# Kernel tuning notes

Hardware: AMD Instinct MI355X
Metric: run time of the kernel (lower is better)

The kernel has to match this reference:

```python
import jax, jax.numpy as jnp
import numpy as np

B, S, E, H = 2, 2048, 1024, 16
D = E // H


def setup_inputs() -> dict:
    key = jax.random.key(0)
    ks = jax.random.split(key, 11)
    def lin(k):
        kw, kb = jax.random.split(k)
        bound = 1.0 / np.sqrt(E)
        W = jax.random.uniform(kw, (E, E), jnp.float32, -bound, bound)
        b = jax.random.uniform(kb, (E,), jnp.float32, -bound, bound)
        return W, b
    Wq, bq = lin(ks[0])
    Wk, bk = lin(ks[1])
    Wv, bv = lin(ks[2])
    Wo, bo = lin(ks[3])
    return {
        "query": jax.random.normal(ks[4], (B, S, E), jnp.float32),
        "key": jax.random.normal(ks[5], (B, S, E), jnp.float32),
        "value": jax.random.normal(ks[6], (B, S, E), jnp.float32),
        "Wq": Wq, "bq": bq, "Wk": Wk, "bk": bk,
        "Wv": Wv, "bv": bv, "Wo": Wo, "bo": bo,
        "is_causal": 1,
    }


def reference(query, key, value, Wq, bq, Wk, bk, Wv, bv, Wo, bo, is_causal):
    scale = D ** -0.5
    def heads(x, W, b):
        # torch Linear: x @ W.T + b, then [B,S,H,D] -> [B,H,S,D]
        y = jnp.einsum('bse,fe->bsf', x, W) + b
        return y.reshape(B, S, H, D).transpose(0, 2, 1, 3)
    q = heads(query, Wq, bq)
    k = heads(key, Wk, bk)
    v = heads(value, Wv, bv)
    scores = jnp.einsum('bhqd,bhkd->bhqk', q, k) * scale  # [B,H,S,S]
    if is_causal:
        mask = jnp.tril(jnp.ones((S, S), dtype=bool))
        scores = jnp.where(mask, scores, -jnp.inf)
    attn = jax.nn.softmax(scores, axis=-1)
    out = jnp.einsum('bhqk,bhkd->bhqd', attn, v)
    out = out.transpose(0, 2, 1, 3).reshape(B, S, E)
    return jnp.einsum('bse,fe->bsf', out, Wo) + bo
```

## Files before the change

kernel.cpp:

```cpp
#include <hip/hip_runtime.h>
#include <cstdint>
#include <cstddef>

typedef unsigned short u16;
typedef unsigned int u32;
typedef __attribute__((ext_vector_type(8))) short bf16x8;
typedef __attribute__((ext_vector_type(4))) float f32x4;
typedef __attribute__((ext_vector_type(16))) float f32x16;
typedef __attribute__((ext_vector_type(4))) u16 u16x4;
typedef __attribute__((ext_vector_type(4))) u32 u32x4;
typedef __attribute__((ext_vector_type(2))) u32 u32x2;

__device__ __forceinline__ u16 f2bf(float f) {
  u32 x = __builtin_bit_cast(u32, f);
  x += 0x7fffu + ((x >> 16) & 1u);
  return (u16)(x >> 16);
}

__device__ __forceinline__ void g2lds16(const u16* g, u16* l) {
  __builtin_amdgcn_global_load_lds(
      (const __attribute__((address_space(1))) u32*)g,
      (__attribute__((address_space(3))) u32*)l, 16, 0, 0);
}

struct CvtArgs { const float* s[7]; u16* d[7]; int n4[7]; };

__global__ __launch_bounds__(256) void cvt_all(CvtArgs a) {
  int y = blockIdx.y;
  const float4* __restrict__ src = (const float4*)a.s[y];
  u16* __restrict__ dst = a.d[y];
  int n4 = a.n4[y];
  for (int i = blockIdx.x * blockDim.x + threadIdx.x; i < n4;
       i += gridDim.x * blockDim.x) {
    float4 v = src[i];
    u16x4 o = { f2bf(v.x), f2bf(v.y), f2bf(v.z), f2bf(v.w) };
    *(u16x4*)(dst + (size_t)i * 4) = o;
  }
}

struct GemmArgs {
  const u16* A[3]; const u16* W[3]; const float* bias[3];
  void* out[3]; float scale[3]; int mode[3];
};

__global__ __launch_bounds__(256) void gemm_fused(GemmArgs ga) {
  __shared__ alignas(16) u16 As[2][128 * 32];
  __shared__ alignas(16) u16 Bs[2][128 * 32];
  const int z = blockIdx.z;
  const u16* __restrict__ A = ga.A[z];
  const u16* __restrict__ W = ga.W[z];
  const int tid = threadIdx.x;
  const int lane = tid & 63;
  const int w = tid >> 6;
  const int lo4 = lane & 15, hi2 = lane >> 4;
  const int l = (int)blockIdx.x + 8 * (int)blockIdx.y;
  const int wl = (l & 7) * 32 + (l >> 3);
  const int m0 = (wl >> 3) * 128;
  const int n0 = (wl & 7) * 128;
  const int wr = w >> 1, wc = w & 1;

  f32x4 acc[4][4] = {};

  auto stage = [&](int kt, int buf) {
    const int k0 = kt * 32;
#pragma unroll
    for (int i = 0; i < 2; ++i) {
      int c = (i * 4 + w) * 64 + lane;
      int r = c >> 2;
      int q = (c & 3) ^ ((r >> 1) & 3);
      g2lds16(A + (size_t)(m0 + r) * 1024 + k0 + q * 8, As[buf] + (i * 4 + w) * 512);
      g2lds16(W + (size_t)(n0 + r) * 1024 + k0 + q * 8, Bs[buf] + (i * 4 + w) * 512);
    }
  };

  stage(0, 0);
  stage(1, 1);
  for (int kt = 0; kt < 32; ++kt) {
    const int cur = kt & 1;
    asm volatile("s_waitcnt vmcnt(4)" ::: "memory");
    __builtin_amdgcn_s_barrier();
    bf16x8 af[4], bfr[4];
#pragma unroll
    for (int i = 0; i < 4; ++i) {
      int r = wr * 64 + i * 16 + lo4;
      int q = hi2 ^ ((r >> 1) & 3);
      af[i] = *(const bf16x8*)(As[cur] + r * 32 + q * 8);
    }
#pragma unroll
    for (int j = 0; j < 4; ++j) {
      int r = wc * 64 + j * 16 + lo4;
      int q = hi2 ^ ((r >> 1) & 3);
      bfr[j] = *(const bf16x8*)(Bs[cur] + r * 32 + q * 8);
    }
#pragma unroll
    for (int i = 0; i < 4; ++i)
#pragma unroll
      for (int j = 0; j < 4; ++j)
        acc[i][j] = __builtin_amdgcn_mfma_f32_16x16x32_bf16(af[i], bfr[j], acc[i][j], 0, 0, 0);
    __builtin_amdgcn_s_barrier();
    stage(kt + 2 < 32 ? kt + 2 : kt, cur);
  }
  asm volatile("s_waitcnt vmcnt(0)" ::: "memory");

  const float* __restrict__ bias = ga.bias[z];
  const float cs = ga.scale[z];
  const int mode = ga.mode[z];
#pragma unroll
  for (int j = 0; j < 4; ++j) {
    int n = n0 + wc * 64 + j * 16 + lo4;
    float bv = bias[n];
#pragma unroll
    for (int i = 0; i < 4; ++i) {
#pragma unroll
      for (int rg = 0; rg < 4; ++rg) {
        int m = m0 + wr * 64 + i * 16 + hi2 * 4 + rg;
        float v = (acc[i][j][rg] + bv) * cs;
        if (mode == 2) {
          ((float*)ga.out[z])[(size_t)m * 1024 + n] = v;
        } else {
          int b = m >> 11, s = m & 2047, h = n >> 6, d = n & 63;
          size_t addr = (mode == 0)
            ? ((size_t)(b * 16 + h) * 2048 + s) * 64 + d
            : ((size_t)(b * 16 + h) * 64 + d) * 2048 + s;
          ((u16*)ga.out[z])[addr] = f2bf(v);
        }
      }
    }
  }
}

__global__ __launch_bounds__(256, 2) void attn_kernel(
    const u16* __restrict__ Q, const u16* __restrict__ K,
    const u16* __restrict__ Vt, u16* __restrict__ Out,
    const int* __restrict__ causal_p) {
  __shared__ alignas(16) u16 Ks[2][2][64 * 64];
  __shared__ alignas(16) u16 Vs[2][2][64 * 64];
  __shared__ float ml2[512];
  const int tid = threadIdx.x, lane = tid & 63, w = tid >> 6;
  const int wg = w >> 1, wv = w & 1;
  const int ql = lane & 31, hi = lane >> 5;
  const int bx = (int)blockIdx.x, by = (int)blockIdx.y;
  const int bh = (bx & 7) * 4 + (by >> 3);
  const int slot = ((bx >> 3) << 3) | (by & 7);
  const int causal = *causal_p;
  const u16* Qb = Q + (size_t)bh * 2048 * 64;
  const u16* Kb = K + (size_t)bh * 2048 * 64;
  const u16* Vb = Vt + (size_t)bh * 64 * 2048;
  const int batch = bh >> 4, h = bh & 15;

  auto stageKV = [&](int jt, int buf) {
#pragma unroll
    for (int i = 0; i < 4; ++i) {
      int c = i * 128 + wv * 64 + lane;
      int r = c >> 3;
      int q = (c & 7) ^ (r & 7);
      g2lds16(Kb + (size_t)(jt * 64 + r) * 64 + q * 8, Ks[wg][buf] + (i * 128 + wv * 64) * 8);
      g2lds16(Vb + (size_t)r * 2048 + jt * 64 + q * 8, Vs[wg][buf] + (i * 128 + wv * 64) * 8);
    }
  };

  float* Od = (float*)&Ks[0][0][0];
  const int li = wv * 64 + lane;

  for (int seg = 0; seg < 2; ++seg) {
    const int qt = seg ? 31 - slot : slot;
    const int qrow = qt * 64 + wv * 32 + ql;

    bf16x8 qf[4];
#pragma unroll
    for (int dsl = 0; dsl < 4; ++dsl)
      qf[dsl] = *(const bf16x8*)(Qb + (size_t)qrow * 64 + dsl * 16 + hi * 8);

    const int nt = causal ? (qt + 1) : 32;
    const int U = (nt + 1) >> 1;

    stageKV(wg, 0);
    stageKV(wg + 2, 1);

    float m_r = -1e30f, l_r = 0.f;
    f32x16 o0 = {}, o1 = {};

    for (int u = 0; u < U; ++u) {
      const int jt = 2 * u + wg;
      const int cur = u & 1;
      asm volatile("s_waitcnt vmcnt(8)" ::: "memory");
      __builtin_amdgcn_s_barrier();

      if (jt < nt) {
        f32x16 s0 = {}, s1 = {};
#pragma unroll
        for (int dsl = 0; dsl < 4; ++dsl) {
          int cc = dsl * 2 + hi;
          bf16x8 k0 = *(const bf16x8*)(Ks[wg][cur] + ql * 64 + ((cc ^ (ql & 7)) * 8));
          bf16x8 k1 = *(const bf16x8*)(Ks[wg][cur] + (32 + ql) * 64 + ((cc ^ (ql & 7)) * 8));
          s0 = __builtin_amdgcn_mfma_f32_32x32x16_bf16(k0, qf[dsl], s0, 0, 0, 0);
          s1 = __builtin_amdgcn_mfma_f32_32x32x16_bf16(k1, qf[dsl], s1, 0, 0, 0);
        }

        if (causal && jt == qt) {
#pragma unroll
          for (int rg = 0; rg < 16; ++rg) {
            int kof = jt * 64 + 8 * (rg >> 2) + (rg & 3) + 4 * hi;
            s0[rg] = (kof > qrow) ? -1e30f : s0[rg];
            s1[rg] = (kof + 32 > qrow) ? -1e30f : s1[rg];
          }
        }

        float pm = fmaxf(s0[0], s1[0]);
#pragma unroll
        for (int rg = 1; rg < 16; ++rg) pm = fmaxf(pm, fmaxf(s0[rg], s1[rg]));
        pm = fmaxf(pm, __shfl_xor(pm, 32));
        if (!__all(pm <= m_r + 8.f)) {
          float mn = fmaxf(m_r, pm);
          float corr = exp2f(m_r - mn);
          m_r = mn; l_r *= corr;
#pragma unroll
          for (int rg = 0; rg < 16; ++rg) { o0[rg] *= corr; o1[rg] *= corr; }
        }
        float sum = 0.f;
#pragma unroll
        for (int rg = 0; rg < 16; ++rg) { s0[rg] = exp2f(s0[rg] - m_r); sum += s0[rg]; }
#pragma unroll
        for (int rg = 0; rg < 16; ++rg) { s1[rg] = exp2f(s1[rg] - m_r); sum += s1[rg]; }
        sum += __shfl_xor(sum, 32);
        l_r += sum;

#pragma unroll
        for (int s = 0; s < 4; ++s) {
          const f32x16& p = (s >= 2) ? s1 : s0;
          const int base = 8 * (s & 1);
          u32 A0, A1, B0, B1;
          asm("v_cvt_pk_bf16_f32 %0, %1, %2" : "=v"(A0) : "v"(p[base + 0]), "v"(p[base + 1]));
          asm("v_cvt_pk_bf16_f32 %0, %1, %2" : "=v"(A1) : "v"(p[base + 2]), "v"(p[base + 3]));
          asm("v_cvt_pk_bf16_f32 %0, %1, %2" : "=v"(B0) : "v"(p[base + 4]), "v"(p[base + 5]));
          asm("v_cvt_pk_bf16_f32 %0, %1, %2" : "=v"(B1) : "v"(p[base + 6]), "v"(p[base + 7]));
          asm volatile("v_permlane32_swap_b32 %0, %1" : "+v"(A0), "+v"(B0));
          asm volatile("v_permlane32_swap_b32 %0, %1" : "+v"(A1), "+v"(B1));
          u32x4 pw = {A0, A1, B0, B1};
          bf16x8 pf = __builtin_bit_cast(bf16x8, pw);
#pragma unroll
          for (int df = 0; df < 2; ++df) {
            int rr = df * 32 + ql;
            bf16x8 vf = *(const bf16x8*)(Vs[wg][cur] + rr * 64 + (((s * 2 + hi) ^ (rr & 7)) * 8));
            if (df) o1 = __builtin_amdgcn_mfma_f32_32x32x16_bf16(vf, pf, o1, 0, 0, 0);
            else    o0 = __builtin_amdgcn_mfma_f32_32x32x16_bf16(vf, pf, o0, 0, 0, 0);
          }
        }
      }
      __builtin_amdgcn_s_barrier();
      stageKV(u + 2 < U ? jt + 4 : jt, cur);
    }
    asm volatile("s_waitcnt vmcnt(0)" ::: "memory");
    __syncthreads();

    if (wg == 1) {
#pragma unroll
      for (int rg = 0; rg < 16; ++rg) {
        Od[li * 33 + rg]      = o0[rg];
        Od[li * 33 + 16 + rg] = o1[rg];
      }
      ml2[li * 3 + 0] = m_r;
      ml2[li * 3 + 1] = l_r;
    }
    __syncthreads();
    if (wg == 0) {
      float m_b = ml2[li * 3 + 0];
      float l_b = ml2[li * 3 + 1];
      float mn = fmaxf(m_r, m_b);
      float ca = exp2f(m_r - mn), cb = exp2f(m_b - mn);
      float rl = 1.f / (l_r * ca + l_b * cb);
      u16* orow = Out + ((size_t)(batch * 2048 + qrow)) * 1024 + h * 64;
#pragma unroll
      for (int df = 0; df < 2; ++df) {
        const f32x16& oo = df ? o1 : o0;
        const float* Op = &Od[li * 33 + df * 16];
#pragma unroll
        for (int b2 = 0; b2 < 4; ++b2) {
          u32 w0, w1;
          float v0 = (oo[4 * b2 + 0] * ca + Op[4 * b2 + 0] * cb) * rl;
          float v1 = (oo[4 * b2 + 1] * ca + Op[4 * b2 + 1] * cb) * rl;
          float v2 = (oo[4 * b2 + 2] * ca + Op[4 * b2 + 2] * cb) * rl;
          float v3 = (oo[4 * b2 + 3] * ca + Op[4 * b2 + 3] * cb) * rl;
          asm("v_cvt_pk_bf16_f32 %0, %1, %2" : "=v"(w0) : "v"(v0), "v"(v1));
          asm("v_cvt_pk_bf16_f32 %0, %1, %2" : "=v"(w1) : "v"(v2), "v"(v3));
          int d0 = df * 32 + b2 * 8 + hi * 4;
          u32x2 pr = {w0, w1};
          *(u32x2*)(orow + d0) = pr;
        }
      }
    }
    __syncthreads();
  }
}

extern "C" void kernel_launch(void* const* d_in, const int* in_sizes, int n_in,
                              void* d_out, int out_size, void* d_ws, size_t ws_size,
                              hipStream_t stream) {
  (void)in_sizes; (void)n_in; (void)out_size; (void)ws_size;
  const float* query = (const float*)d_in[0];
  const float* key   = (const float*)d_in[1];
  const float* value = (const float*)d_in[2];
  const float* Wq = (const float*)d_in[3];
  const float* bq = (const float*)d_in[4];
  const float* Wk = (const float*)d_in[5];
  const float* bk = (const float*)d_in[6];
  const float* Wv = (const float*)d_in[7];
  const float* bv = (const float*)d_in[8];
  const float* Wo = (const float*)d_in[9];
  const float* bo = (const float*)d_in[10];
  const int* is_causal = (const int*)d_in[11];

  u16* wsp = (u16*)d_ws;
  u16* xq  = wsp;
  u16* xk  = xq  + (4u << 20);
  u16* xv  = xk  + (4u << 20);
  u16* wq  = xv  + (4u << 20);
  u16* wk  = wq  + (1u << 20);
  u16* wv  = wk  + (1u << 20);
  u16* wo  = wv  + (1u << 20);
  u16* Qb  = wo  + (1u << 20);
  u16* Kb  = Qb  + (4u << 20);
  u16* Vtb = Kb  + (4u << 20);
  u16* attn= Vtb + (4u << 20);

  CvtArgs ca;
  ca.s[0] = query; ca.d[0] = xq; ca.n4[0] = 1 << 20;
  ca.s[1] = key;   ca.d[1] = xk; ca.n4[1] = 1 << 20;
  ca.s[2] = value; ca.d[2] = xv; ca.n4[2] = 1 << 20;
  ca.s[3] = Wq; ca.d[3] = wq; ca.n4[3] = 1 << 18;
  ca.s[4] = Wk; ca.d[4] = wk; ca.n4[4] = 1 << 18;
  ca.s[5] = Wv; ca.d[5] = wv; ca.n4[5] = 1 << 18;
  ca.s[6] = Wo; ca.d[6] = wo; ca.n4[6] = 1 << 18;
  cvt_all<<<dim3(512, 7), 256, 0, stream>>>(ca);

  const float LOG2E = 1.4426950408889634f;
  GemmArgs g1;
  g1.A[0] = xq; g1.W[0] = wq; g1.bias[0] = bq; g1.out[0] = Qb;
  g1.scale[0] = 0.125f * LOG2E; g1.mode[0] = 0;
  g1.A[1] = xk; g1.W[1] = wk; g1.bias[1] = bk; g1.out[1] = Kb;
  g1.scale[1] = 1.f; g1.mode[1] = 0;
  g1.A[2] = xv; g1.W[2] = wv; g1.bias[2] = bv; g1.out[2] = Vtb;
  g1.scale[2] = 1.f; g1.mode[2] = 1;
  gemm_fused<<<dim3(8, 32, 3), 256, 0, stream>>>(g1);

  attn_kernel<<<dim3(16, 32), 256, 0, stream>>>(Qb, Kb, Vtb, attn, is_causal);

  GemmArgs g2;
  for (int i = 0; i < 3; ++i) {
    g2.A[i] = attn; g2.W[i] = wo; g2.bias[i] = bo; g2.out[i] = d_out;
    g2.scale[i] = 1.f; g2.mode[i] = 2;
  }
  gemm_fused<<<dim3(8, 32, 1), 256, 0, stream>>>(g2);
}
```

Measured before the change: 127.6 us.

## Fuse fp32-to-bf16 activation conversion into QKV projection GEMM

After: 140.3 us. 10.0% more time.

```diff
diff --git a/kernel.cpp b/kernel.cpp
--- a/kernel.cpp
+++ b/kernel.cpp
@@ -22,8 +22,13 @@
       (const __attribute__((address_space(1))) u32*)g,
       (__attribute__((address_space(3))) u32*)l, 16, 0, 0);
 }
-
-struct CvtArgs { const float* s[7]; u16* d[7]; int n4[7]; };
+__device__ __forceinline__ void g2lds16f(const float* g, float* l) {
+  __builtin_amdgcn_global_load_lds(
+      (const __attribute__((address_space(1))) u32*)g,
+      (__attribute__((address_space(3))) u32*)l, 16, 0, 0);
+}
+
+struct CvtArgs { const float* s[4]; u16* d[4]; int n4[4]; };
 
 __global__ __launch_bounds__(256) void cvt_all(CvtArgs a) {
   int y = blockIdx.y;
@@ -124,6 +129,107 @@
             : ((size_t)(b * 16 + h) * 64 + d) * 2048 + s;
           ((u16*)ga.out[z])[addr] = f2bf(v);
         }
+      }
+    }
+  }
+}
+
+struct GemmArgsF {
+  const float* A[3]; const u16* W[3]; const float* bias[3];
+  u16* out[3]; float scale[3]; int mode[3];
+};
+
+__global__ __launch_bounds__(256) void gemm_f32a(GemmArgsF ga) {
+  __shared__ alignas(16) float Af[2][128 * 32];
+  __shared__ alignas(16) u16 Bs[2][128 * 32];
+  const int z = blockIdx.z;
+  const float* __restrict__ A = ga.A[z];
+  const u16* __restrict__ W = ga.W[z];
+  const int tid = threadIdx.x, lane = tid & 63, w = tid >> 6;
+  const int lo4 = lane & 15, hi2 = lane >> 4;
+  const int l = (int)blockIdx.x + 8 * (int)blockIdx.y;
+  const int wl = (l & 7) * 32 + (l >> 3);
+  const int m0 = (wl >> 3) * 128;
+  const int n0 = (wl & 7) * 128;
+  const int wr = w >> 1, wc = w & 1;
+
+  f32x4 acc[4][4] = {};
+
+  auto stage = [&](int kt, int buf) {
+    const int k0 = kt * 32;
+#pragma unroll
+    for (int i = 0; i < 4; ++i) {
+      int c = (i * 4 + w) * 64 + lane;
+      int r = c >> 3;
+      int cc = (c & 7) ^ (r & 7);
+      g2lds16f(A + (size_t)(m0 + r) * 1024 + k0 + cc * 4,
+               Af[buf] + (i * 4 + w) * 256);
+    }
+#pragma unroll
+    for (int i = 0; i < 2; ++i) {
+      int c = (i * 4 + w) * 64 + lane;
+      int r = c >> 2;
+      int q = (c & 3) ^ ((r >> 1) & 3);
+      g2lds16(W + (size_t)(n0 + r) * 1024 + k0 + q * 8, Bs[buf] + (i * 4 + w) * 512);
+    }
+  };
+
+  stage(0, 0);
+  stage(1, 1);
+  for (int kt = 0; kt < 32; ++kt) {
+    const int cur = kt & 1;
+    asm volatile("s_waitcnt vmcnt(6)" ::: "memory");
+    __builtin_amdgcn_s_barrier();
+    bf16x8 af[4], bfr[4];
+#pragma unroll
+    for (int i = 0; i < 4; ++i) {
+      int r = wr * 64 + i * 16 + lo4;
+      int c0 = (2 * hi2) ^ (r & 7);
+      int c1 = (2 * hi2 + 1) ^ (r & 7);
+      float4 fa = *(const float4*)(Af[cur] + r * 32 + c0 * 4);
+      float4 fb = *(const float4*)(Af[cur] + r * 32 + c1 * 4);
+      u32 p0, p1, p2, p3;
+      asm("v_cvt_pk_bf16_f32 %0, %1, %2" : "=v"(p0) : "v"(fa.x), "v"(fa.y));
+      asm("v_cvt_pk_bf16_f32 %0, %1, %2" : "=v"(p1) : "v"(fa.z), "v"(fa.w));
+      asm("v_cvt_pk_bf16_f32 %0, %1, %2" : "=v"(p2) : "v"(fb.x), "v"(fb.y));
+      asm("v_cvt_pk_bf16_f32 %0, %1, %2" : "=v"(p3) : "v"(fb.z), "v"(fb.w));
+      u32x4 pw = {p0, p1, p2, p3};
+      af[i] = __builtin_bit_cast(bf16x8, pw);
+    }
+#pragma unroll
+    for (int j = 0; j < 4; ++j) {
+      int r = wc * 64 + j * 16 + lo4;
+      int q = hi2 ^ ((r >> 1) & 3);
+      bfr[j] = *(const bf16x8*)(Bs[cur] + r * 32 + q * 8);
+    }
+#pragma unroll
+    for (int i = 0; i < 4; ++i)
+#pragma unroll
+      for (int j = 0; j < 4; ++j)
+        acc[i][j] = __builtin_amdgcn_mfma_f32_16x16x32_bf16(af[i], bfr[j], acc[i][j], 0, 0, 0);
+    __builtin_amdgcn_s_barrier();
+    stage(kt + 2 < 32 ? kt + 2 : kt, cur);
+  }
+  asm volatile("s_waitcnt vmcnt(0)" ::: "memory");
+
+  const float* __restrict__ bias = ga.bias[z];
+  const float cs = ga.scale[z];
+  const int mode = ga.mode[z];
+#pragma unroll
+  for (int j = 0; j < 4; ++j) {
+    int n = n0 + wc * 64 + j * 16 + lo4;
+    float bv = bias[n];
+#pragma unroll
+    for (int i = 0; i < 4; ++i) {
+#pragma unroll
+      for (int rg = 0; rg < 4; ++rg) {
+        int m = m0 + wr * 64 + i * 16 + hi2 * 4 + rg;
+        float v = (acc[i][j][rg] + bv) * cs;
+        int b = m >> 11, s = m & 2047, h = n >> 6, d = n & 63;
+        size_t addr = (mode == 0)
+          ? ((size_t)(b * 16 + h) * 2048 + s) * 64 + d
+          : ((size_t)(b * 16 + h) * 64 + d) * 2048 + s;
+        ga.out[z][addr] = f2bf(v);
       }
     }
   }
@@ -324,24 +430,21 @@
   u16* attn= Vtb + (4u << 20);
 
   CvtArgs ca;
-  ca.s[0] = query; ca.d[0] = xq; ca.n4[0] = 1 << 20;
-  ca.s[1] = key;   ca.d[1] = xk; ca.n4[1] = 1 << 20;
-  ca.s[2] = value; ca.d[2] = xv; ca.n4[2] = 1 << 20;
-  ca.s[3] = Wq; ca.d[3] = wq; ca.n4[3] = 1 << 18;
-  ca.s[4] = Wk; ca.d[4] = wk; ca.n4[4] = 1 << 18;
-  ca.s[5] = Wv; ca.d[5] = wv; ca.n4[5] = 1 << 18;
-  ca.s[6] = Wo; ca.d[6] = wo; ca.n4[6] = 1 << 18;
-  cvt_all<<<dim3(512, 7), 256, 0, stream>>>(ca);
+  ca.s[0] = Wq; ca.d[0] = wq; ca.n4[0] = 1 << 18;
+  ca.s[1] = Wk; ca.d[1] = wk; ca.n4[1] = 1 << 18;
+  ca.s[2] = Wv; ca.d[2] = wv; ca.n4[2] = 1 << 18;
+  ca.s[3] = Wo; ca.d[3] = wo; ca.n4[3] = 1 << 18;
+  cvt_all<<<dim3(256, 4), 256, 0, stream>>>(ca);
 
   const float LOG2E = 1.4426950408889634f;
-  GemmArgs g1;
-  g1.A[0] = xq; g1.W[0] = wq; g1.bias[0] = bq; g1.out[0] = Qb;
+  GemmArgsF g1;
+  g1.A[0] = query; g1.W[0] = wq; g1.bias[0] = bq; g1.out[0] = Qb;
   g1.scale[0] = 0.125f * LOG2E; g1.mode[0] = 0;
-  g1.A[1] = xk; g1.W[1] = wk; g1.bias[1] = bk; g1.out[1] = Kb;
+  g1.A[1] = key;   g1.W[1] = wk; g1.bias[1] = bk; g1.out[1] = Kb;
   g1.scale[1] = 1.f; g1.mode[1] = 0;
-  g1.A[2] = xv; g1.W[2] = wv; g1.bias[2] = bv; g1.out[2] = Vtb;
+  g1.A[2] = value; g1.W[2] = wv; g1.bias[2] = bv; g1.out[2] = Vtb;
   g1.scale[2] = 1.f; g1.mode[2] = 1;
-  gemm_fused<<<dim3(8, 32, 3), 256, 0, stream>>>(g1);
+  gemm_f32a<<<dim3(8, 32, 3), 256, 0, stream>>>(g1);
 
   attn_kernel<<<dim3(16, 32), 256, 0, stream>>>(Qb, Kb, Vtb, attn, is_causal);
 
```
